# Optimization experiments

Hardware: AMD Instinct MI355X
Metric: run time of the kernel (lower is better)

The kernel has to match this reference:

```python
import jax, jax.numpy as jnp
import numpy as np

BN_EPS = 1e-5


def _conv(x, w, b):
    # x [B,C,H,W], w [O,I,kh,kw], VALID padding, stride 1
    out = jax.lax.conv_general_dilated(x, w, (1, 1), 'VALID',
                                       dimension_numbers=('NCHW', 'OIHW', 'NCHW'))
    return out + b[None, :, None, None]


def _bilinear(img, y, x):
    # img [B,C,H,W]; y,x [B,K,Ho,Wo] fractional sample coords; zero outside.
    B, C, H, W = img.shape
    y0 = jnp.floor(y); x0 = jnp.floor(x)
    y1 = y0 + 1.0;     x1 = x0 + 1.0
    wy1 = y - y0; wy0 = 1.0 - wy1
    wx1 = x - x0; wx0 = 1.0 - wx1
    bidx = jnp.arange(B)[:, None, None, None]

    def g(yi, xi, wgt):
        valid = (yi >= 0) & (yi <= H - 1) & (xi >= 0) & (xi <= W - 1)
        yc = jnp.clip(yi, 0, H - 1).astype(jnp.int32)
        xc = jnp.clip(xi, 0, W - 1).astype(jnp.int32)
        v = img[bidx, :, yc, xc]  # [B,K,Ho,Wo,C]
        return v * (wgt * valid)[..., None]

    return (g(y0, x0, wy0 * wx0) + g(y0, x1, wy0 * wx1)
            + g(y1, x0, wy1 * wx0) + g(y1, x1, wy1 * wx1))


def _dcn_out(x, w_off, b_off, w_dcn, b_dcn, gamma, beta):
    k = w_dcn.shape[2]          # kernel height (kernel = (k,1))
    pad = k // 2
    # F.pad([0,0,pad,pad]): pad H only
    xp = jnp.pad(x, ((0, 0), (0, 0), (pad, pad), (0, 0)))
    B, C, Hp, W = xp.shape
    Ho = Hp - k + 1             # == original H for odd k
    Wo = W
    # offset/mask conv: 3*k output channels (dy | dx | mask)
    om = _conv(xp, w_off, b_off)                  # [B,3k,Ho,Wo]
    dy, dx = om[:, :k], om[:, k:2 * k]
    mask = jax.nn.sigmoid(om[:, 2 * k:])          # [B,k,Ho,Wo]
    # sample coordinates: base grid + per-tap offset
    y = (jnp.arange(Ho, dtype=x.dtype)[None, None, :, None]
         + jnp.arange(k, dtype=x.dtype)[None, :, None, None] + dy)
    xc = jnp.arange(Wo, dtype=x.dtype)[None, None, None, :] + dx
    sampled = _bilinear(xp, y, xc) * mask[..., None]   # [B,k,Ho,Wo,C]
    out = jnp.einsum('bkhwc,ock->bohw', sampled, w_dcn[:, :, :, 0])
    out = out + b_dcn[None, :, None, None]
    # BatchNorm2d (training-mode batch statistics) + ReLU
    mean = out.mean(axis=(0, 2, 3), keepdims=True)
    var = out.var(axis=(0, 2, 3), keepdims=True)
    out = (out - mean) * jax.lax.rsqrt(var + BN_EPS)
    out = out * gamma[None, :, None, None] + beta[None, :, None, None]
    return jax.nn.relu(out)


def setup_inputs() -> dict:
    key = jax.random.key(0)
    ks = jax.random.split(key, 6)
    B, C, H, W, k = 8, 64, 256, 256, 3
    x = jax.random.normal(ks[0], (B, C, H, W), dtype=jnp.float32)
    fan = C * k
    w_off = jax.random.normal(ks[1], (3 * k, C, k, 1), dtype=jnp.float32) * 0.01
    b_off = jnp.zeros((3 * k,), dtype=jnp.float32)
    w_dcn = jax.random.normal(ks[2], (C, C, k, 1), dtype=jnp.float32) / np.sqrt(fan)
    b_dcn = jax.random.normal(ks[3], (C,), dtype=jnp.float32) * 0.01
    gamma = jnp.ones((C,), dtype=jnp.float32)
    beta = jnp.zeros((C,), dtype=jnp.float32)
    return {'x': x, 'w_off': w_off, 'b_off': b_off, 'w_dcn': w_dcn,
            'b_dcn': b_dcn, 'gamma': gamma, 'beta': beta}


def reference(x, w_off, b_off, w_dcn, b_dcn, gamma, beta):
    return _dcn_out(x, w_off, b_off, w_dcn, b_dcn, gamma, beta)
```

## Files before the change

### kernel.cpp

```cpp
#include <hip/hip_runtime.h>
#include <cmath>

#define HW 65536
#define NPER 524288
#define NBLK 8192

typedef _Float16 f16;
typedef __attribute__((ext_vector_type(8))) _Float16 f16x8;
typedef __attribute__((ext_vector_type(4))) float f32x4;

__device__ __forceinline__ f16x8 splat8(f16 h) {
  f16x8 r = {h, h, h, h, h, h, h, h};
  return r;
}

#define SUMS_OFF  0
#define WTO_OFF   128
#define WTH_OFF   1664
#define PART_OFF  7808
#define XT_OFF    1056384
#define OUT16_OFF 17833600

__global__ __launch_bounds__(256) void prep_wts(
    const float* __restrict__ w_off, const float* __restrict__ w_dcn,
    f16* __restrict__ wtO, f16* __restrict__ wtH) {
  int i = blockIdx.x * 256 + threadIdx.x;
  if (i < 12288) {
    int o = i / 192, k = i - o * 192, kh = k >> 6, c = k & 63;
    wtH[i] = (f16)w_dcn[(o * 64 + c) * 3 + kh];
  }
  if (i < 3072) {
    int n = i / 192, k = i - n * 192, kh = k >> 6, c = k & 63;
    wtO[i] = (n < 9) ? (f16)w_off[(n * 64 + c) * 3 + kh] : (f16)0.f;
  }
}

__global__ __launch_bounds__(256) void xpose(
    const float* __restrict__ x, f16* __restrict__ xT) {
  int t = threadIdx.x, lane = t & 63, cq = t >> 6;
  int blk = blockIdx.x;
  int b = blk >> 10;
  int rem = blk & 1023;
  int h = rem >> 2, w0 = (rem & 3) << 6;
  int w = w0 + lane, c0 = cq << 4;
  const float* xb = x + (((size_t)b) << 6) * HW + (size_t)h * 256 + w;
  float v[16];
#pragma unroll
  for (int j = 0; j < 16; ++j) v[j] = xb[(size_t)(c0 + j) * HW];
  f16x8 a, bb;
#pragma unroll
  for (int j = 0; j < 8; ++j) { a[j] = (f16)v[j]; bb[j] = (f16)v[8 + j]; }
  f16* dst = xT + (((size_t)b * HW + (size_t)h * 256 + w) << 6) + c0;
  *(f16x8*)dst = a;
  *(f16x8*)(dst + 8) = bb;
}

__global__ __launch_bounds__(256, 5) void dcn_fused(
    const f16* __restrict__ xT, const f16* __restrict__ wtO,
    const float* __restrict__ b_off, const f16* __restrict__ wtH,
    const float* __restrict__ b_dcn, f16* __restrict__ out16,
    float* __restrict__ part) {
  __shared__ __align__(16) unsigned char lds[30208];
  f16*   sA   = (f16*)lds;
  float* sOut = (float*)lds;
  float* sOM  = (float*)(lds + 25600);
  unsigned short* sWo = (unsigned short*)(lds + 25600);
  f16*   sWw  = (f16*)(lds + 27136);

  const int t = threadIdx.x, lane = t & 63, cq = t >> 6;
  const int c0 = cq << 4;
  const int lrow = lane & 15, lq = lane >> 4, kgrp = lq << 3;
  const int pix8 = lane >> 3, chunk = lane & 7;
  const int cb8 = chunk << 3;

  int g = ((blockIdx.x & 7) << 10) | (blockIdx.x >> 3);
  int b = g >> 10;
  int rem = g & 1023;
  int h = rem >> 2, w0 = (rem & 3) << 6;
  const f16* xb = xT + (((size_t)b * HW) << 6);

  f16x8 Ac[6];
#pragma unroll
  for (int kt = 0; kt < 6; ++kt) {
    int hr = h + (kt >> 1) - 1;
    int hc = min(max(hr, 0), 255);
    int cb = ((kt & 1) << 5) + kgrp;
    const f16* src = xb + (((size_t)(hc * 256 + w0 + c0 + lrow)) << 6) + cb;
    f16x8 v = *(const f16x8*)src;
    if (!(hr >= 0 && hr < 256)) v = splat8((f16)0.f);
    Ac[kt] = v;
  }
  f32x4 accO = {0.f, 0.f, 0.f, 0.f};
#pragma unroll
  for (int kt = 0; kt < 6; ++kt) {
    f16x8 Bo = *(const f16x8*)(wtO + lrow * 192 + kt * 32 + kgrp);
    accO = __builtin_amdgcn_mfma_f32_16x16x32_f16(Ac[kt], Bo, accO, 0, 0, 0);
  }
  float boffv = (lrow < 9) ? b_off[lrow] : 0.f;
#pragma unroll
  for (int r = 0; r < 4; ++r)
    sOM[(c0 + lq * 4 + r) * 17 + lrow] = accO[r] + boffv;
  __syncthreads();

  float dy = 0.f, dxv = 0.f, mpre = 0.f;
  int px = t & 63, khw = t >> 6;
  if (t < 192) {
    dy   = sOM[px * 17 + khw];
    dxv  = sOM[px * 17 + 3 + khw];
    mpre = sOM[px * 17 + 6 + khw];
  }
  __syncthreads();
  if (t < 192) {
    float m = 1.f / (1.f + __expf(-mpre));
    float yf = (float)(h + khw) + dy;
    float xf = (float)(w0 + px) + dxv;
    float y0f = floorf(yf), x0f = floorf(xf);
    int iy0 = (int)y0f, ix0 = (int)x0f;
    float wy1 = yf - y0f, wy0 = 1.f - wy1;
    float wx1 = xf - x0f, wx0 = 1.f - wx1;
    int r0 = iy0 - 1, r1 = iy0, g0 = ix0, g1 = ix0 + 1;
    bool vr0 = (r0 >= 0) & (r0 < 256), vr1 = (r1 >= 0) & (r1 < 256);
    bool vc0 = (g0 >= 0) & (g0 < 256), vc1 = (g1 >= 0) & (g1 < 256);
    float w00 = (vr0 & vc0) ? wy0 * wx0 * m : 0.f;
    float w01 = (vr0 & vc1) ? wy0 * wx1 * m : 0.f;
    float w10 = (vr1 & vc0) ? wy1 * wx0 * m : 0.f;
    float w11 = (vr1 & vc1) ? wy1 * wx1 * m : 0.f;
    int e = px * 3 + khw;
    sWo[e * 4 + 0] = (unsigned short)min(max(r0, 0), 255);
    sWo[e * 4 + 1] = (unsigned short)min(max(r1, 0), 255);
    sWo[e * 4 + 2] = (unsigned short)min(max(g0, 0), 255);
    sWo[e * 4 + 3] = (unsigned short)min(max(g1, 0), 255);
    sWw[e * 4 + 0] = (f16)w00;
    sWw[e * 4 + 1] = (f16)w01;
    sWw[e * 4 + 2] = (f16)w10;
    sWw[e * 4 + 3] = (f16)w11;
  }
  __syncthreads();

#pragma unroll
  for (int kh = 0; kh < 3; ++kh) {
#pragma unroll
    for (int half = 0; half < 2; ++half) {
      int pix = c0 + half * 8 + pix8;
      int e = pix * 3 + kh;
      unsigned short r0 = sWo[e * 4 + 0], r1 = sWo[e * 4 + 1];
      unsigned short g0 = sWo[e * 4 + 2], g1 = sWo[e * 4 + 3];
      f16 w00 = sWw[e * 4 + 0], w01 = sWw[e * 4 + 1];
      f16 w10 = sWw[e * 4 + 2], w11 = sWw[e * 4 + 3];
      const f16* p00 = xb + ((((int)r0 << 8) + g0) << 6) + cb8;
      const f16* p01 = xb + ((((int)r0 << 8) + g1) << 6) + cb8;
      const f16* p10 = xb + ((((int)r1 << 8) + g0) << 6) + cb8;
      const f16* p11 = xb + ((((int)r1 << 8) + g1) << 6) + cb8;
      f16x8 a00 = *(const f16x8*)p00;
      f16x8 a01 = *(const f16x8*)p01;
      f16x8 a10 = *(const f16x8*)p10;
      f16x8 a11 = *(const f16x8*)p11;
      f16x8 s = a00 * splat8(w00) + a01 * splat8(w01) +
                a10 * splat8(w10) + a11 * splat8(w11);
      *(f16x8*)(sA + pix * 200 + kh * 64 + cb8) = s;
    }
  }

  const int nrow = c0 + lrow;
  f16x8 Bf[6];
#pragma unroll
  for (int kt = 0; kt < 6; ++kt)
    Bf[kt] = *(const f16x8*)(wtH + nrow * 192 + kt * 32 + kgrp);
  float bdc = b_dcn[nrow];
  __syncthreads();

  f32x4 acc[4];
#pragma unroll
  for (int mt = 0; mt < 4; ++mt) acc[mt] = (f32x4){0.f, 0.f, 0.f, 0.f};
#pragma unroll
  for (int kt = 0; kt < 6; ++kt) {
#pragma unroll
    for (int mt = 0; mt < 4; ++mt) {
      f16x8 Af = *(const f16x8*)(sA + (mt * 16 + lrow) * 200 + kt * 32 + kgrp);
      acc[mt] = __builtin_amdgcn_mfma_f32_16x16x32_f16(Af, Bf[kt], acc[mt],
                                                       0, 0, 0);
    }
  }
  __syncthreads();

  float s1 = 0.f, s2 = 0.f;
#pragma unroll
  for (int mt = 0; mt < 4; ++mt) {
    int prow = mt * 16 + lq * 4;
    f32x4 vv;
#pragma unroll
    for (int r = 0; r < 4; ++r) {
      float v = acc[mt][r] + bdc;
      vv[r] = v;
      s1 += v;
      s2 += v * v;
    }
    *(f32x4*)(sOut + nrow * 66 + prow) = vv;
  }
  s1 += __shfl_xor(s1, 16); s1 += __shfl_xor(s1, 32);
  s2 += __shfl_xor(s2, 16); s2 += __shfl_xor(s2, 32);
  if (lq == 0) {
    part[(size_t)nrow * NBLK + blockIdx.x] = s1;
    part[(size_t)(64 + nrow) * NBLK + blockIdx.x] = s2;
  }
  __syncthreads();

  f16* ob = out16 + (((size_t)b) << 6) * HW + (size_t)h * 256 + w0;
#pragma unroll
  for (int i = 0; i < 16; ++i) {
    int o = c0 + i;
    ob[(size_t)o * HW + lane] = (f16)sOut[o * 66 + lane];
  }
}

__global__ __launch_bounds__(256) void reduce_sums(
    const float* __restrict__ part, float* __restrict__ sums) {
  int j = blockIdx.x;
  const float4* p4 = (const float4*)(part + (size_t)j * NBLK);
  float s = 0.f;
  for (int i = threadIdx.x; i < NBLK / 4; i += 256) {
    float4 v = p4[i];
    s += v.x + v.y + v.z + v.w;
  }
#pragma unroll
  for (int off = 32; off > 0; off >>= 1) s += __shfl_down(s, off);
  __shared__ float ls[4];
  int wid = threadIdx.x >> 6, ln = threadIdx.x & 63;
  if (ln == 0) ls[wid] = s;
  __syncthreads();
  if (threadIdx.x == 0) sums[j] = ls[0] + ls[1] + ls[2] + ls[3];
}

__global__ __launch_bounds__(256) void bn_apply(
    const f16* __restrict__ out16, float* __restrict__ out,
    const float* __restrict__ sums, const float* __restrict__ gamma,
    const float* __restrict__ beta) {
  int blk = blockIdx.x;
  int pl = blk >> 2, q = blk & 3;
  int o = pl & 63;
  float mean = sums[o] * (1.f / (float)NPER);
  float var = sums[64 + o] * (1.f / (float)NPER) - mean * mean;
  float inv = rsqrtf(var + 1e-5f);
  float sc = gamma[o] * inv;
  float sh = beta[o] - mean * sc;
  const f16x8* src = (const f16x8*)(out16 + (size_t)pl * HW + q * 16384);
  float4* dst = (float4*)(out + (size_t)pl * HW + q * 16384);
  for (int i = threadIdx.x; i < 2048; i += 256) {
    f16x8 v = src[i];
    float4 lo, hi;
    lo.x = fmaxf(fmaf((float)v[0], sc, sh), 0.f);
    lo.y = fmaxf(fmaf((float)v[1], sc, sh), 0.f);
    lo.z = fmaxf(fmaf((float)v[2], sc, sh), 0.f);
    lo.w = fmaxf(fmaf((float)v[3], sc, sh), 0.f);
    hi.x = fmaxf(fmaf((float)v[4], sc, sh), 0.f);
    hi.y = fmaxf(fmaf((float)v[5], sc, sh), 0.f);
    hi.z = fmaxf(fmaf((float)v[6], sc, sh), 0.f);
    hi.w = fmaxf(fmaf((float)v[7], sc, sh), 0.f);
    dst[2 * i] = lo;
    dst[2 * i + 1] = hi;
  }
}

extern "C" void kernel_launch(void* const* d_in, const int* in_sizes, int n_in,
                              void* d_out, int out_size, void* d_ws, size_t ws_size,
                              hipStream_t stream) {
  const float* x     = (const float*)d_in[0];
  const float* w_off = (const float*)d_in[1];
  const float* b_off = (const float*)d_in[2];
  const float* w_dcn = (const float*)d_in[3];
  const float* b_dcn = (const float*)d_in[4];
  const float* gamma = (const float*)d_in[5];
  const float* beta  = (const float*)d_in[6];
  float* out = (float*)d_out;
  float* ws  = (float*)d_ws;

  float* sums = ws + SUMS_OFF;
  f16*   wtO  = (f16*)(ws + WTO_OFF);
  f16*   wtH  = (f16*)(ws + WTH_OFF);
  float* part = ws + PART_OFF;
  f16*   xT   = (f16*)(ws + XT_OFF);
  f16*   o16  = (f16*)(ws + OUT16_OFF);

  prep_wts<<<48, 256, 0, stream>>>(w_off, w_dcn, wtO, wtH);
  xpose<<<8192, 256, 0, stream>>>(x, xT);
  dcn_fused<<<NBLK, 256, 0, stream>>>(xT, wtO, b_off, wtH, b_dcn, o16, part);
  reduce_sums<<<128, 256, 0, stream>>>(part, sums);
  bn_apply<<<2048, 256, 0, stream>>>(o16, out, sums, gamma, beta);
}
```

Before: 384.8 us.

## Coalesce transpose stores via LDS, batch gather loads, and restructure partial-sum reduction

The transpose kernel now stages converted values in shared memory, so each thread writes 32 contiguous bytes of a pixel's channel vector instead of scattered 16-byte stores. In the fused kernel, all 24 bilinear gather loads are issued before any arithmetic, which gives more memory-level parallelism at the cost of extra registers. Per-block statistics are written as one contiguous 128-float row, and the reduction kernel sums them column-wise and accumulates into zero-initialised sums with atomics. The extra register pressure could lower occupancy under the 5-blocks launch bound.

```diff
diff --git a/kernel.cpp b/kernel.cpp
--- a/kernel.cpp
+++ b/kernel.cpp
@@ -7,6 +7,7 @@
 
 typedef _Float16 f16;
 typedef __attribute__((ext_vector_type(8))) _Float16 f16x8;
+typedef __attribute__((ext_vector_type(4))) _Float16 f16x4;
 typedef __attribute__((ext_vector_type(4))) float f32x4;
 
 __device__ __forceinline__ f16x8 splat8(f16 h) {
@@ -23,8 +24,9 @@
 
 __global__ __launch_bounds__(256) void prep_wts(
     const float* __restrict__ w_off, const float* __restrict__ w_dcn,
-    f16* __restrict__ wtO, f16* __restrict__ wtH) {
+    f16* __restrict__ wtO, f16* __restrict__ wtH, float* __restrict__ sums) {
   int i = blockIdx.x * 256 + threadIdx.x;
+  if (i < 128) sums[i] = 0.f;
   if (i < 12288) {
     int o = i / 192, k = i - o * 192, kh = k >> 6, c = k & 63;
     wtH[i] = (f16)w_dcn[(o * 64 + c) * 3 + kh];
@@ -37,22 +39,30 @@
 
 __global__ __launch_bounds__(256) void xpose(
     const float* __restrict__ x, f16* __restrict__ xT) {
+  __shared__ f16 sX[64 * 68];
   int t = threadIdx.x, lane = t & 63, cq = t >> 6;
   int blk = blockIdx.x;
   int b = blk >> 10;
   int rem = blk & 1023;
   int h = rem >> 2, w0 = (rem & 3) << 6;
-  int w = w0 + lane, c0 = cq << 4;
-  const float* xb = x + (((size_t)b) << 6) * HW + (size_t)h * 256 + w;
+  int c0 = cq << 4;
+  const float* xb = x + (((size_t)b) << 6) * HW + (size_t)h * 256 + w0 + lane;
   float v[16];
 #pragma unroll
   for (int j = 0; j < 16; ++j) v[j] = xb[(size_t)(c0 + j) * HW];
   f16x8 a, bb;
 #pragma unroll
   for (int j = 0; j < 8; ++j) { a[j] = (f16)v[j]; bb[j] = (f16)v[8 + j]; }
-  f16* dst = xT + (((size_t)b * HW + (size_t)h * 256 + w) << 6) + c0;
-  *(f16x8*)dst = a;
-  *(f16x8*)(dst + 8) = bb;
+  f16* d = sX + lane * 68 + c0;
+  *(f16x8*)d = a;
+  *(f16x8*)(d + 8) = bb;
+  __syncthreads();
+  int px = t >> 2, c16 = (t & 3) << 4;
+  f16x8 o0 = *(const f16x8*)(sX + px * 68 + c16);
+  f16x8 o1 = *(const f16x8*)(sX + px * 68 + c16 + 8);
+  f16* dst = xT + (((size_t)b * HW + (size_t)h * 256 + w0 + px) << 6) + c16;
+  *(f16x8*)dst = o0;
+  *(f16x8*)(dst + 8) = o1;
 }
 
 __global__ __launch_bounds__(256, 5) void dcn_fused(
@@ -66,6 +76,7 @@
   float* sOM  = (float*)(lds + 25600);
   unsigned short* sWo = (unsigned short*)(lds + 25600);
   f16*   sWw  = (f16*)(lds + 27136);
+  float* sP   = (float*)(lds + 27136);
 
   const int t = threadIdx.x, lane = t & 63, cq = t >> 6;
   const int c0 = cq << 4;
@@ -137,28 +148,35 @@
   }
   __syncthreads();
 
-#pragma unroll
-  for (int kh = 0; kh < 3; ++kh) {
-#pragma unroll
-    for (int half = 0; half < 2; ++half) {
-      int pix = c0 + half * 8 + pix8;
-      int e = pix * 3 + kh;
-      unsigned short r0 = sWo[e * 4 + 0], r1 = sWo[e * 4 + 1];
-      unsigned short g0 = sWo[e * 4 + 2], g1 = sWo[e * 4 + 3];
-      f16 w00 = sWw[e * 4 + 0], w01 = sWw[e * 4 + 1];
-      f16 w10 = sWw[e * 4 + 2], w11 = sWw[e * 4 + 3];
-      const f16* p00 = xb + ((((int)r0 << 8) + g0) << 6) + cb8;
-      const f16* p01 = xb + ((((int)r0 << 8) + g1) << 6) + cb8;
-      const f16* p10 = xb + ((((int)r1 << 8) + g0) << 6) + cb8;
-      const f16* p11 = xb + ((((int)r1 << 8) + g1) << 6) + cb8;
-      f16x8 a00 = *(const f16x8*)p00;
-      f16x8 a01 = *(const f16x8*)p01;
-      f16x8 a10 = *(const f16x8*)p10;
-      f16x8 a11 = *(const f16x8*)p11;
-      f16x8 s = a00 * splat8(w00) + a01 * splat8(w01) +
-                a10 * splat8(w10) + a11 * splat8(w11);
-      *(f16x8*)(sA + pix * 200 + kh * 64 + cb8) = s;
-    }
+  ushort4 po[6];
+  f16x4  wv[6];
+#pragma unroll
+  for (int i = 0; i < 6; ++i) {
+    int kh = i >> 1, half = i & 1;
+    int e = (c0 + half * 8 + pix8) * 3 + kh;
+    po[i] = *(const ushort4*)(sWo + e * 4);
+    wv[i] = *(const f16x4*)(sWw + e * 4);
+  }
+  f16x8 gv[24];
+#pragma unroll
+  for (int i = 0; i < 6; ++i) {
+    int b00 = (((int)po[i].x << 8) + (int)po[i].z) << 6;
+    int b01 = (((int)po[i].x << 8) + (int)po[i].w) << 6;
+    int b10 = (((int)po[i].y << 8) + (int)po[i].z) << 6;
+    int b11 = (((int)po[i].y << 8) + (int)po[i].w) << 6;
+    gv[i * 4 + 0] = *(const f16x8*)(xb + b00 + cb8);
+    gv[i * 4 + 1] = *(const f16x8*)(xb + b01 + cb8);
+    gv[i * 4 + 2] = *(const f16x8*)(xb + b10 + cb8);
+    gv[i * 4 + 3] = *(const f16x8*)(xb + b11 + cb8);
+  }
+#pragma unroll
+  for (int i = 0; i < 6; ++i) {
+    int kh = i >> 1, half = i & 1;
+    f16x8 s = gv[i * 4 + 0] * splat8(wv[i][0]) +
+              gv[i * 4 + 1] * splat8(wv[i][1]) +
+              gv[i * 4 + 2] * splat8(wv[i][2]) +
+              gv[i * 4 + 3] * splat8(wv[i][3]);
+    *(f16x8*)(sA + (c0 + half * 8 + pix8) * 200 + kh * 64 + cb8) = s;
   }
 
   const int nrow = c0 + lrow;
@@ -200,11 +218,12 @@
   s1 += __shfl_xor(s1, 16); s1 += __shfl_xor(s1, 32);
   s2 += __shfl_xor(s2, 16); s2 += __shfl_xor(s2, 32);
   if (lq == 0) {
-    part[(size_t)nrow * NBLK + blockIdx.x] = s1;
-    part[(size_t)(64 + nrow) * NBLK + blockIdx.x] = s2;
-  }
-  __syncthreads();
-
+    sP[nrow] = s1;
+    sP[64 + nrow] = s2;
+  }
+  __syncthreads();
+
+  if (t < 128) part[(size_t)blockIdx.x * 128 + t] = sP[t];
   f16* ob = out16 + (((size_t)b) << 6) * HW + (size_t)h * 256 + w0;
 #pragma unroll
   for (int i = 0; i < 16; ++i) {
@@ -215,20 +234,17 @@
 
 __global__ __launch_bounds__(256) void reduce_sums(
     const float* __restrict__ part, float* __restrict__ sums) {
-  int j = blockIdx.x;
-  const float4* p4 = (const float4*)(part + (size_t)j * NBLK);
+  int r = blockIdx.x;
+  int j = threadIdx.x & 127, half = threadIdx.x >> 7;
+  const float* p = part + ((size_t)r * 64 + half * 32) * 128 + j;
   float s = 0.f;
-  for (int i = threadIdx.x; i < NBLK / 4; i += 256) {
-    float4 v = p4[i];
-    s += v.x + v.y + v.z + v.w;
-  }
-#pragma unroll
-  for (int off = 32; off > 0; off >>= 1) s += __shfl_down(s, off);
-  __shared__ float ls[4];
-  int wid = threadIdx.x >> 6, ln = threadIdx.x & 63;
-  if (ln == 0) ls[wid] = s;
-  __syncthreads();
-  if (threadIdx.x == 0) sums[j] = ls[0] + ls[1] + ls[2] + ls[3];
+#pragma unroll
+  for (int i = 0; i < 32; ++i) s += p[(size_t)i * 128];
+  __shared__ float ls[256];
+  ls[threadIdx.x] = s;
+  __syncthreads();
+  if (threadIdx.x < 128)
+    atomicAdd(&sums[threadIdx.x], ls[threadIdx.x] + ls[128 + threadIdx.x]);
 }
 
 __global__ __launch_bounds__(256) void bn_apply(
@@ -281,7 +297,7 @@
   f16*   xT   = (f16*)(ws + XT_OFF);
   f16*   o16  = (f16*)(ws + OUT16_OFF);
 
-  prep_wts<<<48, 256, 0, stream>>>(w_off, w_dcn, wtO, wtH);
+  prep_wts<<<48, 256, 0, stream>>>(w_off, w_dcn, wtO, wtH, sums);
   xpose<<<8192, 256, 0, stream>>>(x, xT);
   dcn_fused<<<NBLK, 256, 0, stream>>>(xT, wtO, b_off, wtH, b_dcn, o16, part);
   reduce_sums<<<128, 256, 0, stream>>>(part, sums);
```

New measurement: 375.1 us. -2.5%, faster.
